# Performance work log

Measured on AMD Instinct MI355X. Metric: run time of the kernel, lower is better.

## Reference

```python
import jax, jax.numpy as jnp
import numpy as np

B, N, D, H = 128, 512, 128, 8
DK = D // H
CLIP = 10.0                      # tanh_clipping
NORM = float(np.sqrt(D))         # norm_factor = sqrt(embedding_dim), used as multiplier (as in source)


def setup_inputs() -> dict:
    key = jax.random.key(0)
    ks = jax.random.split(key, 7)
    std = float(1.0 / np.sqrt(D))
    return {
        "embeddings": jax.random.normal(ks[0], (B, N, D), dtype=jnp.float32),
        "eval_seq": jax.random.randint(ks[1], (B, N), 0, N, dtype=jnp.int32),
        "W_placeholder": jax.random.uniform(ks[2], (2 * D,), jnp.float32, -std, std),
        "W_node": jax.random.normal(ks[3], (D, 3 * D), jnp.float32) * std,
        "W_fixed": jax.random.normal(ks[4], (D, D), jnp.float32) * std,
        "W_step": jax.random.normal(ks[5], (2 * D, D), jnp.float32) * std,
        "W_out": jax.random.normal(ks[6], (D, D), jnp.float32) * std,
    }


def _decode(embeddings, eval_seq, W_placeholder, W_node, W_fixed, W_step, W_out):
    # Precomputed (fixed) projections, as in the torch module before the decode loop
    proj = embeddings @ W_node                                  # [B,N,3D]
    gK, gV, lK = jnp.split(proj, 3, axis=-1)
    gK = gK.reshape(B, N, H, DK).transpose(2, 0, 1, 3)          # [H,B,N,dk]
    gV = gV.reshape(B, N, H, DK).transpose(2, 0, 1, 3)          # [H,B,N,dk]
    fixed = embeddings.mean(axis=1) @ W_fixed                   # [B,D]
    batch_ix = jnp.arange(B)

    def step_logp(ctx, mask):
        # ctx: [B,2D] step context; mask: [B,N] bool (True = visited)
        query = fixed + ctx @ W_step                            # [B,D]
        qh = query.reshape(B, H, DK)
        compat = NORM * jnp.einsum('bhd,hbnd->hbn', qh, gK)     # [H,B,N]
        compat = jnp.where(mask[None], -jnp.inf, compat)        # mask_inner
        attn = jax.nn.softmax(compat, axis=-1)
        heads = jnp.einsum('hbn,hbnd->hbd', attn, gV)           # [H,B,dk]
        glimpse = heads.transpose(1, 0, 2).reshape(B, D) @ W_out
        logits = NORM * jnp.einsum('bnd,bd->bn', lK, glimpse)   # [B,N]
        logits = jnp.tanh(logits) * CLIP
        logits = jnp.where(mask, -jnp.inf, logits)              # mask_logits
        return jax.nn.log_softmax(logits, axis=-1)              # temp = 1.0

    # step 0: W_placeholder context, empty mask
    mask0 = jnp.zeros((B, N), dtype=bool)
    ctx0 = jnp.broadcast_to(W_placeholder[None, :], (B, 2 * D))
    lp0 = step_logp(ctx0, mask0)
    sel0 = eval_seq[:, 0]
    mask1 = mask0.at[batch_ix, sel0].set(True)
    emb_first = embeddings[batch_ix, sel0]                      # [B,D] (constant across steps)

    def body(carry, sel_i):
        mask, last = carry
        ctx = jnp.concatenate([emb_first, embeddings[batch_ix, last]], axis=-1)  # [B,2D]
        lp = step_logp(ctx, mask)
        new_mask = mask.at[batch_ix, sel_i].set(True)           # update mask AFTER computing log_p
        return (new_mask, sel_i), lp

    (_, _), lps = jax.lax.scan(body, (mask1, sel0), eval_seq[:, 1:].T)  # lps: [N-1,B,N]
    log_p = jnp.concatenate([lp0[None], lps], axis=0).transpose(1, 0, 2)  # [B,N,N]
    return log_p


def reference(embeddings, eval_seq, W_placeholder, W_node, W_fixed, W_step, W_out):
    log_p = _decode(embeddings, eval_seq, W_placeholder, W_node, W_fixed, W_step, W_out)
    return log_p, eval_seq
```

## Files before the change

### kernel.cpp

```cpp
#include <hip/hip_runtime.h>
#include <math.h>

#define B_ 128
#define N_ 512
#define D_ 128
#define H_ 8
#define NORM_ 11.313708498984761f
#define SC_ 16.322324f
#define HSC_ 32.644648f
#define CLIP_ 10.0f
#define MASKC_ -3.0e38f
#define NEG_BIG_ -1.0e30f
#define L2E_ 1.4426950408889634f
#define LN2_ 0.6931471805599453f

typedef unsigned short ushortx;
typedef __attribute__((ext_vector_type(8))) short s8v;
typedef __attribute__((ext_vector_type(4))) float f4v;

#define MFMA_ __builtin_amdgcn_mfma_f32_16x16x32_bf16

__device__ __forceinline__ unsigned short f2bf(float x) {
  union { float f; unsigned u; } v; v.f = x;
  unsigned r = v.u + 0x7fffu + ((v.u >> 16) & 1u);
  return (unsigned short)(r >> 16);
}
__device__ __forceinline__ float bf2f(ushortx u) {
  union { unsigned u; float f; } v; v.u = ((unsigned)u) << 16; return v.f;
}
__device__ __forceinline__ unsigned cvtpk(float lo, float hi) {
  unsigned r;
  asm("v_cvt_pk_bf16_f32 %0, %1, %2" : "=v"(r) : "v"(lo), "v"(hi));
  return r;
}
__device__ __forceinline__ float exp2_hw(float x) {
  float r; asm("v_exp_f32 %0, %1" : "=v"(r) : "v"(x)); return r;
}
__device__ __forceinline__ float log2_hw(float x) {
  float r; asm("v_log_f32 %0, %1" : "=v"(r) : "v"(x)); return r;
}
__device__ __forceinline__ float rcp_hw(float x) {
  float r; asm("v_rcp_f32 %0, %1" : "=v"(r) : "v"(x)); return r;
}
__device__ __forceinline__ float max3f(float a, float b, float c) {
  float r; asm("v_max3_f32 %0, %1, %2, %3" : "=v"(r) : "v"(a), "v"(b), "v"(c));
  return r;
}

__global__ __launch_bounds__(512)
void prologue(const float* __restrict__ emb, const int* __restrict__ seq,
              const float* __restrict__ Wp, const float* __restrict__ Wnode,
              const float* __restrict__ Wfix, const float* __restrict__ Wstep,
              const float* __restrict__ Wout,
              ushortx* __restrict__ WfT, ushortx* __restrict__ WsbT,
              ushortx* __restrict__ Ksrt, ushortx* __restrict__ n_orig,
              ushortx* __restrict__ Qb0, float* __restrict__ Abuf,
              float* __restrict__ out, int tail_count) {
  const int blk = blockIdx.x;
  const int t = threadIdx.x;

  if (blk < 128) {
    const int c = blk * 4 + (t >> 7);
    const int k = t & 127;
    if (c < 256) {
      WfT[c * 128 + k] = f2bf(Wnode[k * 384 + c]);
    } else if (c < 384) {
      const int d = c - 256;
      float s = 0.f;
      #pragma unroll 4
      for (int j = 0; j < 128; ++j) s += Wnode[k * 384 + 256 + j] * Wout[d * 128 + j];
      WfT[c * 128 + k] = f2bf(s);
    } else {
      const int d = c - 384;
      WsbT[d * 128 + k] = f2bf(Wstep[(128 + k) * 128 + d] * SC_);
    }
    return;
  }

  if (blk < 256) {
    const int b = blk - 128;
    const int lane = t & 63, wv = t >> 6;
    __shared__ int Tl[512];
    __shared__ int wsum[8];
    __shared__ int tot_s;

    Tl[t] = 0x7fffffff;
    __syncthreads();
    const int node = seq[b * 512 + t];
    atomicMin(&Tl[node], t + 1);
    __syncthreads();

    const int f = (Tl[node] == t + 1) ? 1 : 0;
    const unsigned long long bal = __ballot(f);
    const int excl = __popcll(bal & ((1ull << lane) - 1ull));
    if (lane == 0) wsum[wv] = __popcll(bal);
    __syncthreads();
    int woff = 0;
    #pragma unroll
    for (int i = 0; i < 8; ++i) woff += (i < wv) ? wsum[i] : 0;
    const int Kt = woff + excl;
    Ksrt[b * 512 + t] = (ushortx)Kt;
    if (f) n_orig[b * 512 + Kt] = (ushortx)node;
    if (t == 511) tot_s = Kt + f;

    const int g = (Tl[t] == 0x7fffffff) ? 1 : 0;
    const unsigned long long bal2 = __ballot(g);
    const int excl2 = __popcll(bal2 & ((1ull << lane) - 1ull));
    const int w2 = __popcll(bal2);
    __syncthreads();
    if (lane == 0) wsum[wv] = w2;
    __syncthreads();
    int woff2 = 0;
    #pragma unroll
    for (int i = 0; i < 8; ++i) woff2 += (i < wv) ? wsum[i] : 0;
    if (g) n_orig[b * 512 + tot_s + woff2 + excl2] = (ushortx)t;
    return;
  }

  if (blk < 384) {
    const int b = blk - 256;
    __shared__ float4 red4[16][33];
    __shared__ float mean[128];
    const int row0 = t >> 5, c4 = t & 31;
    const float* eb = emb + (size_t)b * 512 * 128;
    float4 acc = {0.f, 0.f, 0.f, 0.f};
    for (int it = 0; it < 32; ++it) {
      const float4 x = *(const float4*)(eb + (size_t)(it * 16 + row0) * 128 + c4 * 4);
      acc.x += x.x; acc.y += x.y; acc.z += x.z; acc.w += x.w;
    }
    red4[row0][c4] = acc;
    __syncthreads();
    if (t < 128) {
      const int c4b = t >> 2, j = t & 3;
      float s = 0.f;
      #pragma unroll
      for (int r = 0; r < 16; ++r) s += ((const float*)&red4[r][c4b])[j];
      mean[t] = s * (1.f / 512.f);
    }
    __syncthreads();
    if (t < 128) {
      float fx = 0.f;
      for (int k = 0; k < 128; ++k) fx += mean[k] * Wfix[k * 128 + t];
      float c = 0.f;
      for (int k = 0; k < 256; ++k) c += Wp[k] * Wstep[k * 128 + t];
      const int sel0 = seq[b * N_];
      const float* ef = eb + (size_t)sel0 * 128;
      float a = 0.f;
      for (int k = 0; k < 128; ++k) a += ef[k] * Wstep[k * 128 + t];
      Qb0[b * 128 + t] = f2bf((fx + c) * SC_);
      Abuf[b * 128 + t] = (fx + a) * SC_;
    }
    return;
  }

  {
    const int i = (blk - 384) * 512 + t;
    if (i < tail_count) out[(size_t)B_ * N_ * N_ + i] = (float)seq[i];
  }
}

__global__ __launch_bounds__(256)
void proj_mfma(const float* __restrict__ E, const ushortx* __restrict__ WfT,
               const ushortx* __restrict__ n_orig,
               ushortx* __restrict__ gK, ushortx* __restrict__ gVt,
               ushortx* __restrict__ lKt) {
  __shared__ ushortx S[64 * 216];
  const int tid = threadIdx.x;
  const int w = tid >> 6, l = tid & 63;
  const int m16 = l & 15, lg = l >> 4;
  const int b = blockIdx.x >> 3;
  const int n0 = (blockIdx.x & 7) * 64;
  const int p_row = n0 + w * 16 + m16;
  const int orig = (int)n_orig[b * 512 + p_row];
  const float* er = E + ((size_t)b * 512 + orig) * 128;

  s8v af[4];
  #pragma unroll
  for (int ks = 0; ks < 4; ++ks) {
    float4 f0 = *(const float4*)(er + ks * 32 + lg * 8);
    float4 f1 = *(const float4*)(er + ks * 32 + lg * 8 + 4);
    union { unsigned u[4]; s8v v; } au;
    au.u[0] = cvtpk(f0.x, f0.y); au.u[1] = cvtpk(f0.z, f0.w);
    au.u[2] = cvtpk(f1.x, f1.y); au.u[3] = cvtpk(f1.z, f1.w);
    af[ks] = au.v;
  }

  const int lrow = w * 16 + 4 * lg;
  #pragma unroll
  for (int half = 0; half < 2; ++half) {
    const int cb = half * 192;
    #pragma unroll
    for (int ct = 0; ct < 12; ++ct) {
      const int lc = ct * 16 + m16;
      f4v acc = {0.f, 0.f, 0.f, 0.f};
      #pragma unroll
      for (int ks = 0; ks < 4; ++ks) {
        const s8v bf = *(const s8v*)(WfT + (size_t)(cb + lc) * 128 + ks * 32 + lg * 8);
        acc = MFMA_(af[ks], bf, acc, 0, 0, 0);
      }
      const unsigned w01 = cvtpk(acc[0], acc[1]);
      const unsigned w23 = cvtpk(acc[2], acc[3]);
      S[(lrow + 0) * 216 + lc] = (ushortx)(w01 & 0xffffu);
      S[(lrow + 1) * 216 + lc] = (ushortx)(w01 >> 16);
      S[(lrow + 2) * 216 + lc] = (ushortx)(w23 & 0xffffu);
      S[(lrow + 3) * 216 + lc] = (ushortx)(w23 >> 16);
    }
    __syncthreads();

    if (half == 0) {
      #pragma unroll
      for (int it = 0; it < 4; ++it) {
        const int idx = it * 256 + tid;
        const int hh = idx >> 7, nn = (idx >> 1) & 63, hf = idx & 1;
        const uint4 v = *(const uint4*)(&S[nn * 216 + hh * 16 + hf * 8]);
        *(uint4*)(gK + (((size_t)(b * 8 + hh) * 512 + n0 + nn) * 16 + hf * 8)) = v;
      }
      #pragma unroll
      for (int it = 0; it < 2; ++it) {
        const int idx = it * 256 + tid;
        const int hh = idx >> 7, dk = (idx >> 3) & 15, n8 = (idx & 7) * 8;
        const int lc = 128 + hh * 16 + dk;
        unsigned wr[4];
        #pragma unroll
        for (int j = 0; j < 4; ++j)
          wr[j] = (unsigned)S[(n8 + 2 * j) * 216 + lc] |
                  ((unsigned)S[(n8 + 2 * j + 1) * 216 + lc] << 16);
        uint4 o; o.x = wr[0]; o.y = wr[1]; o.z = wr[2]; o.w = wr[3];
        *(uint4*)(gVt + (((size_t)(b * 8 + hh) * 16 + dk) * 512 + n0 + n8)) = o;
      }
    } else {
      #pragma unroll
      for (int it = 0; it < 4; ++it) {
        const int idx = it * 256 + tid;
        const int nn = idx >> 4, d8 = (idx & 15) * 8;
        const uint4 v = *(const uint4*)(&S[nn * 216 + 64 + d8]);
        *(uint4*)(lKt + ((size_t)(b * 512 + n0 + nn) * 128 + d8)) = v;
      }
      #pragma unroll
      for (int it = 0; it < 2; ++it) {
        const int idx = it * 256 + tid;
        const int hq = idx >> 7, dk = (idx >> 3) & 15, n8 = (idx & 7) * 8;
        const int lc = hq * 16 + dk;
        unsigned wr[4];
        #pragma unroll
        for (int j = 0; j < 4; ++j)
          wr[j] = (unsigned)S[(n8 + 2 * j) * 216 + lc] |
                  ((unsigned)S[(n8 + 2 * j + 1) * 216 + lc] << 16);
        uint4 o; o.x = wr[0]; o.y = wr[1]; o.z = wr[2]; o.w = wr[3];
        *(uint4*)(gVt + (((size_t)(b * 8 + 4 + hq) * 16 + dk) * 512 + n0 + n8)) = o;
      }
    }
    __syncthreads();
  }
}

__global__ __launch_bounds__(512, 8)
void decode_mfma(const ushortx* __restrict__ gK,
                 const ushortx* __restrict__ gVt,
                 const ushortx* __restrict__ lKt,
                 const float* __restrict__ emb,
                 const int* __restrict__ seq,
                 const ushortx* __restrict__ WsbT,
                 const float* __restrict__ Abuf,
                 const ushortx* __restrict__ Qb0,
                 const ushortx* __restrict__ Ksrt,
                 const ushortx* __restrict__ n_orig,
                 float* __restrict__ out) {
  const int id = blockIdx.x;
  const int xcd = id & 7, pos = id >> 3;
  const int b = xcd * 16 + (pos >> 5);
  const int s0 = (pos & 31) * 16;
  const int tid = threadIdx.x;
  const int w = tid >> 6, l = tid & 63;
  const int m16 = l & 15, lg = l >> 4;

  __shared__ ushortx logitsTb[512 * 26];
  __shared__ ushortx ctxh[16][136];
  __shared__ ushortx Qt[16][136];
  __shared__ ushortx norig_l[512];
  __shared__ ushortx Ko[16];
  __shared__ int sel_l[16];
  __shared__ float Ab[128];

  norig_l[tid] = n_orig[b * 512 + tid];
  if (tid < 16) {
    Ko[tid] = Ksrt[b * 512 + s0 + tid];
    const int sg = s0 + tid;
    sel_l[tid] = (sg >= 1) ? seq[b * 512 + sg - 1] : 0;
  }
  if (tid < 128) Ab[tid] = Abuf[b * 128 + tid];
  __syncthreads();

  if (tid < 256) {
    const int row = tid >> 4, c8 = (tid & 15) * 8;
    const float* er = emb + ((size_t)b * 512 + sel_l[row]) * 128 + c8;
    float4 f0 = *(const float4*)(er);
    float4 f1 = *(const float4*)(er + 4);
    unsigned* dst = (unsigned*)&ctxh[row][c8];
    dst[0] = cvtpk(f0.x, f0.y); dst[1] = cvtpk(f0.z, f0.w);
    dst[2] = cvtpk(f1.x, f1.y); dst[3] = cvtpk(f1.z, f1.w);
  }
  __syncthreads();

  const int h = w;
  {
    s8v aw[4];
    #pragma unroll
    for (int ks = 0; ks < 4; ++ks)
      aw[ks] = *(const s8v*)(WsbT + (size_t)(h * 16 + m16) * 128 + ks * 32 + lg * 8);
    f4v acc = {0.f, 0.f, 0.f, 0.f};
    #pragma unroll
    for (int ks = 0; ks < 4; ++ks) {
      const s8v bf = *(const s8v*)(&ctxh[m16][ks * 32 + lg * 8]);
      acc = MFMA_(aw[ks], bf, acc, 0, 0, 0);
    }
    const int d0 = h * 16 + 4 * lg;
    unsigned q01 = cvtpk(acc[0] + Ab[d0], acc[1] + Ab[d0 + 1]);
    unsigned q23 = cvtpk(acc[2] + Ab[d0 + 2], acc[3] + Ab[d0 + 3]);
    if (s0 == 0 && m16 == 0) {
      q01 = *(const unsigned*)(Qb0 + b * 128 + d0);
      q23 = *(const unsigned*)(Qb0 + b * 128 + d0 + 2);
    }
    unsigned* qdst = (unsigned*)&Qt[m16][d0];
    qdst[0] = q01; qdst[1] = q23;
  }
  __syncthreads();

  s8v qf = {};
  if (lg < 2) qf = *(const s8v*)(&Qt[m16][h * 16 + lg * 8]);

  s8v ones;
  {
    union { unsigned u[4]; s8v v; } ou;
    ou.u[0] = 0x3F803F80u; ou.u[1] = 0x3F803F80u;
    ou.u[2] = 0x3F803F80u; ou.u[3] = 0x3F803F80u;
    ones = ou.v;
  }

  const int K0i = (int)Ko[0], K15 = (int)Ko[15];
  const int chStart = K0i >> 5;
  const int chClean = (K15 + 31) >> 5;
  const int Ks = (int)Ko[m16];
  const size_t bh = (size_t)(b * 8 + h);

  f4v Oacc = {0.f, 0.f, 0.f, 0.f};
  f4v Lacc = {0.f, 0.f, 0.f, 0.f};
  float m_run = NEG_BIG_;
  const int nA0 = 8 * (m16 >> 2) + (m16 & 3);

  for (int ch = chStart; ch < 16; ++ch) {
    const int base = ch * 32;
    s8v a0 = {}, a1 = {};
    if (lg < 2) {
      a0 = *(const s8v*)(gK + ((bh * 512 + base + nA0) * 16 + lg * 8));
      a1 = *(const s8v*)(gK + ((bh * 512 + base + nA0 + 4) * 16 + lg * 8));
    }
    const s8v av = *(const s8v*)(gVt + ((bh * 16 + m16) * 512 + base + lg * 8));

    f4v z = {0.f, 0.f, 0.f, 0.f};
    f4v st0 = MFMA_(a0, qf, z, 0, 0, 0);
    f4v st1 = MFMA_(a1, qf, z, 0, 0, 0);

    float cm = max3f(st0[0], st0[1], st0[2]);
    cm = max3f(cm, st0[3], st1[0]);
    cm = max3f(cm, st1[1], st1[2]);
    cm = fmaxf(cm, st1[3]);
    cm = fmaxf(cm, __shfl_xor(cm, 16));
    cm = fmaxf(cm, __shfl_xor(cm, 32));

    if (__any(cm > m_run + 8.0f)) {
      const float mn = fmaxf(m_run, cm);
      const float cr = exp2_hw(m_run - mn);
      m_run = mn;
      Lacc[0] *= cr;
      Oacc[0] *= cr; Oacc[1] *= cr; Oacc[2] *= cr; Oacc[3] *= cr;
    }

    float p[8];
    #pragma unroll
    for (int r = 0; r < 4; ++r) {
      p[r]     = exp2_hw(st0[r] - m_run);
      p[4 + r] = exp2_hw(st1[r] - m_run);
    }
    if (ch < chClean) {
      const int nb = base + 8 * lg;
      #pragma unroll
      for (int j = 0; j < 8; ++j) p[j] = (nb + j < Ks) ? 0.f : p[j];
    }
    union { unsigned u[4]; s8v v; } pu;
    pu.u[0] = cvtpk(p[0], p[1]); pu.u[1] = cvtpk(p[2], p[3]);
    pu.u[2] = cvtpk(p[4], p[5]); pu.u[3] = cvtpk(p[6], p[7]);
    Oacc = MFMA_(av, pu.v, Oacc, 0, 0, 0);
    Lacc = MFMA_(ones, pu.v, Lacc, 0, 0, 0);
  }

  const float scale = rcp_hw(Lacc[0]) * HSC_;
  {
    const int d0 = h * 16 + 4 * lg;
    unsigned* hd = (unsigned*)&ctxh[m16][d0];
    hd[0] = cvtpk(Oacc[0] * scale, Oacc[1] * scale);
    hd[1] = cvtpk(Oacc[2] * scale, Oacc[3] * scale);
  }
  __syncthreads();

  #pragma unroll
  for (int nt = 0; nt < 4; ++nt) {
    const int n0 = w * 64 + nt * 16;
    const int pb = (n0 + 4 * lg) * 26 + m16;
    if (n0 + 16 <= K0i) {
      logitsTb[pb]      = f2bf(MASKC_);
      logitsTb[pb + 26] = f2bf(MASKC_);
      logitsTb[pb + 52] = f2bf(MASKC_);
      logitsTb[pb + 78] = f2bf(MASKC_);
      continue;
    }
    f4v acc = {0.f, 0.f, 0.f, 0.f};
    #pragma unroll
    for (int ks = 0; ks < 4; ++ks) {
      const s8v aL = *(const s8v*)(lKt + ((size_t)b * 512 + n0 + m16) * 128 + ks * 32 + lg * 8);
      const s8v bH = *(const s8v*)(&ctxh[m16][ks * 32 + lg * 8]);
      acc = MFMA_(aL, bH, acc, 0, 0, 0);
    }
    const bool bnd = (n0 < K15);
    float lgv[4];
    #pragma unroll
    for (int r = 0; r < 4; ++r) {
      const int p = n0 + 4 * lg + r;
      float x = fminf(fmaxf(acc[r], -43.f), 43.f);
      const float e2 = exp2_hw(x);
      float lv = CLIP_ * (e2 - 1.f) * rcp_hw(e2 + 1.f);
      if (bnd && p < Ks) lv = MASKC_;
      lgv[r] = lv;
    }
    const unsigned pk01 = cvtpk(lgv[0], lgv[1]);
    const unsigned pk23 = cvtpk(lgv[2], lgv[3]);
    logitsTb[pb]      = (ushortx)pk01;
    logitsTb[pb + 26] = (ushortx)(pk01 >> 16);
    logitsTb[pb + 52] = (ushortx)pk23;
    logitsTb[pb + 78] = (ushortx)(pk23 >> 16);
  }
  __syncthreads();

  int no[8];
  #pragma unroll
  for (int i = 0; i < 8; ++i) no[i] = (int)norig_l[i * 64 + l];
  #pragma unroll
  for (int pass = 0; pass < 2; ++pass) {
    const int s = w + pass * 8;
    float v[8];
    #pragma unroll
    for (int i = 0; i < 8; ++i) v[i] = bf2f(logitsTb[(i * 64 + l) * 26 + s]);
    float mm = max3f(v[0], v[1], v[2]);
    mm = max3f(mm, v[3], v[4]);
    mm = max3f(mm, v[5], v[6]);
    mm = fmaxf(mm, v[7]);
    #pragma unroll
    for (int off = 1; off <= 32; off <<= 1) mm = fmaxf(mm, __shfl_xor(mm, off));
    float es = 0.f;
    #pragma unroll
    for (int i = 0; i < 8; ++i) es += exp2_hw((v[i] - mm) * L2E_);
    #pragma unroll
    for (int off = 1; off <= 32; off <<= 1) es += __shfl_xor(es, off);
    const float logZ = mm + LN2_ * log2_hw(es);
    float* orow = out + ((size_t)(b * N_ + s0 + s)) * N_;
    #pragma unroll
    for (int i = 0; i < 8; ++i)
      orow[no[i]] = fmaxf(v[i] - logZ, NEG_BIG_);
  }
}

extern "C" void kernel_launch(void* const* d_in, const int* in_sizes, int n_in,
                              void* d_out, int out_size, void* d_ws, size_t ws_size,
                              hipStream_t stream) {
  const float* emb   = (const float*)d_in[0];
  const int*   seq   = (const int*)d_in[1];
  const float* Wp    = (const float*)d_in[2];
  const float* Wnode = (const float*)d_in[3];
  const float* Wfix  = (const float*)d_in[4];
  const float* Wstep = (const float*)d_in[5];
  const float* Wout  = (const float*)d_in[6];
  float* out = (float*)d_out;

  ushortx* gK    = (ushortx*)d_ws;
  ushortx* gVt   = gK   + (size_t)8388608;
  ushortx* lKt   = gVt  + (size_t)8388608;
  ushortx* WfT   = lKt  + (size_t)8388608;
  ushortx* WsbT  = WfT  + (size_t)49152;
  ushortx* Ksrt  = WsbT + (size_t)16384;
  ushortx* n_or  = Ksrt + (size_t)65536;
  ushortx* Qb0   = n_or + (size_t)65536;
  float*   Abuf  = (float*)(Qb0 + (size_t)16384);

  const long long lp_elems = (long long)B_ * N_ * N_;
  const int tail = (int)((long long)out_size - lp_elems);

  prologue<<<512, 512, 0, stream>>>(emb, seq, Wp, Wnode, Wfix, Wstep, Wout,
                                    WfT, WsbT, Ksrt, n_or, Qb0, Abuf,
                                    out, tail > 0 ? tail : 0);
  proj_mfma<<<1024, 256, 0, stream>>>(emb, WfT, n_or, gK, gVt, lKt);
  decode_mfma<<<4096, 512, 0, stream>>>(gK, gVt, lKt, emb, seq, WsbT, Abuf,
                                        Qb0, Ksrt, n_or, out);
}
```

Measured before the change: 238.3 us.

## Process 32 decode steps per block to reuse gK/gV/lK loads

Each decode block now handles 32 query steps instead of 16. Every gK/gVt chunk loaded in the attention loop feeds two independent online-softmax accumulators, and the lKt tiles are reused for both halves of the logits phase. This halves the grid and the global traffic for keys and values per step. In exchange each block does twice the serial work, holds more registers, uses more shared memory and adds barriers. The attention loop also starts at the first half's start chunk, so the second half loses some of the chunk skipping it had before.

After: 224.7 us, median of 3. 5.7% less time.

```diff
diff --git a/kernel.cpp b/kernel.cpp
--- a/kernel.cpp
+++ b/kernel.cpp
@@ -268,22 +268,22 @@
                  float* __restrict__ out) {
   const int id = blockIdx.x;
   const int xcd = id & 7, pos = id >> 3;
-  const int b = xcd * 16 + (pos >> 5);
-  const int s0 = (pos & 31) * 16;
+  const int b = xcd * 16 + (pos >> 4);
+  const int s0 = (pos & 15) * 32;
   const int tid = threadIdx.x;
   const int w = tid >> 6, l = tid & 63;
   const int m16 = l & 15, lg = l >> 4;
 
   __shared__ ushortx logitsTb[512 * 26];
-  __shared__ ushortx ctxh[16][136];
-  __shared__ ushortx Qt[16][136];
+  __shared__ ushortx ctxh[32][136];
+  __shared__ ushortx Qt[32][136];
   __shared__ ushortx norig_l[512];
-  __shared__ ushortx Ko[16];
-  __shared__ int sel_l[16];
+  __shared__ ushortx Ko[32];
+  __shared__ int sel_l[32];
   __shared__ float Ab[128];
 
   norig_l[tid] = n_orig[b * 512 + tid];
-  if (tid < 16) {
+  if (tid < 32) {
     Ko[tid] = Ksrt[b * 512 + s0 + tid];
     const int sg = s0 + tid;
     sel_l[tid] = (sg >= 1) ? seq[b * 512 + sg - 1] : 0;
@@ -291,7 +291,7 @@
   if (tid < 128) Ab[tid] = Abuf[b * 128 + tid];
   __syncthreads();
 
-  if (tid < 256) {
+  {
     const int row = tid >> 4, c8 = (tid & 15) * 8;
     const float* er = emb + ((size_t)b * 512 + sel_l[row]) * 128 + c8;
     float4 f0 = *(const float4*)(er);
@@ -308,26 +308,32 @@
     #pragma unroll
     for (int ks = 0; ks < 4; ++ks)
       aw[ks] = *(const s8v*)(WsbT + (size_t)(h * 16 + m16) * 128 + ks * 32 + lg * 8);
-    f4v acc = {0.f, 0.f, 0.f, 0.f};
-    #pragma unroll
-    for (int ks = 0; ks < 4; ++ks) {
-      const s8v bf = *(const s8v*)(&ctxh[m16][ks * 32 + lg * 8]);
-      acc = MFMA_(aw[ks], bf, acc, 0, 0, 0);
-    }
-    const int d0 = h * 16 + 4 * lg;
-    unsigned q01 = cvtpk(acc[0] + Ab[d0], acc[1] + Ab[d0 + 1]);
-    unsigned q23 = cvtpk(acc[2] + Ab[d0 + 2], acc[3] + Ab[d0 + 3]);
-    if (s0 == 0 && m16 == 0) {
-      q01 = *(const unsigned*)(Qb0 + b * 128 + d0);
-      q23 = *(const unsigned*)(Qb0 + b * 128 + d0 + 2);
-    }
-    unsigned* qdst = (unsigned*)&Qt[m16][d0];
-    qdst[0] = q01; qdst[1] = q23;
+    #pragma unroll
+    for (int t = 0; t < 2; ++t) {
+      f4v acc = {0.f, 0.f, 0.f, 0.f};
+      #pragma unroll
+      for (int ks = 0; ks < 4; ++ks) {
+        const s8v bf = *(const s8v*)(&ctxh[t * 16 + m16][ks * 32 + lg * 8]);
+        acc = MFMA_(aw[ks], bf, acc, 0, 0, 0);
+      }
+      const int d0 = h * 16 + 4 * lg;
+      unsigned q01 = cvtpk(acc[0] + Ab[d0], acc[1] + Ab[d0 + 1]);
+      unsigned q23 = cvtpk(acc[2] + Ab[d0 + 2], acc[3] + Ab[d0 + 3]);
+      if (s0 == 0 && t == 0 && m16 == 0) {
+        q01 = *(const unsigned*)(Qb0 + b * 128 + d0);
+        q23 = *(const unsigned*)(Qb0 + b * 128 + d0 + 2);
+      }
+      unsigned* qdst = (unsigned*)&Qt[t * 16 + m16][d0];
+      qdst[0] = q01; qdst[1] = q23;
+    }
   }
   __syncthreads();
 
-  s8v qf = {};
-  if (lg < 2) qf = *(const s8v*)(&Qt[m16][h * 16 + lg * 8]);
+  s8v qfA = {}, qfB = {};
+  if (lg < 2) {
+    qfA = *(const s8v*)(&Qt[m16][h * 16 + lg * 8]);
+    qfB = *(const s8v*)(&Qt[16 + m16][h * 16 + lg * 8]);
+  }
 
   s8v ones;
   {
@@ -337,15 +343,17 @@
     ones = ou.v;
   }
 
-  const int K0i = (int)Ko[0], K15 = (int)Ko[15];
-  const int chStart = K0i >> 5;
-  const int chClean = (K15 + 31) >> 5;
-  const int Ks = (int)Ko[m16];
+  const int K0A = (int)Ko[0], K15 = (int)Ko[15];
+  const int K0B = (int)Ko[16], K31 = (int)Ko[31];
+  const int chStart = K0A >> 5;
+  const int chCleanA = (K15 + 31) >> 5;
+  const int chCleanB = (K31 + 31) >> 5;
+  const int KsA = (int)Ko[m16], KsB = (int)Ko[16 + m16];
   const size_t bh = (size_t)(b * 8 + h);
 
-  f4v Oacc = {0.f, 0.f, 0.f, 0.f};
-  f4v Lacc = {0.f, 0.f, 0.f, 0.f};
-  float m_run = NEG_BIG_;
+  f4v OA = {0.f, 0.f, 0.f, 0.f}, OB = {0.f, 0.f, 0.f, 0.f};
+  f4v LA = {0.f, 0.f, 0.f, 0.f}, LB = {0.f, 0.f, 0.f, 0.f};
+  float mA = NEG_BIG_, mB = NEG_BIG_;
   const int nA0 = 8 * (m16 >> 2) + (m16 & 3);
 
   for (int ch = chStart; ch < 16; ++ch) {
@@ -356,116 +364,160 @@
       a1 = *(const s8v*)(gK + ((bh * 512 + base + nA0 + 4) * 16 + lg * 8));
     }
     const s8v av = *(const s8v*)(gVt + ((bh * 16 + m16) * 512 + base + lg * 8));
+    const int nb = base + 8 * lg;
 
     f4v z = {0.f, 0.f, 0.f, 0.f};
-    f4v st0 = MFMA_(a0, qf, z, 0, 0, 0);
-    f4v st1 = MFMA_(a1, qf, z, 0, 0, 0);
-
-    float cm = max3f(st0[0], st0[1], st0[2]);
-    cm = max3f(cm, st0[3], st1[0]);
-    cm = max3f(cm, st1[1], st1[2]);
-    cm = fmaxf(cm, st1[3]);
-    cm = fmaxf(cm, __shfl_xor(cm, 16));
-    cm = fmaxf(cm, __shfl_xor(cm, 32));
-
-    if (__any(cm > m_run + 8.0f)) {
-      const float mn = fmaxf(m_run, cm);
-      const float cr = exp2_hw(m_run - mn);
-      m_run = mn;
-      Lacc[0] *= cr;
-      Oacc[0] *= cr; Oacc[1] *= cr; Oacc[2] *= cr; Oacc[3] *= cr;
-    }
-
-    float p[8];
-    #pragma unroll
-    for (int r = 0; r < 4; ++r) {
-      p[r]     = exp2_hw(st0[r] - m_run);
-      p[4 + r] = exp2_hw(st1[r] - m_run);
-    }
-    if (ch < chClean) {
-      const int nb = base + 8 * lg;
-      #pragma unroll
-      for (int j = 0; j < 8; ++j) p[j] = (nb + j < Ks) ? 0.f : p[j];
-    }
-    union { unsigned u[4]; s8v v; } pu;
-    pu.u[0] = cvtpk(p[0], p[1]); pu.u[1] = cvtpk(p[2], p[3]);
-    pu.u[2] = cvtpk(p[4], p[5]); pu.u[3] = cvtpk(p[6], p[7]);
-    Oacc = MFMA_(av, pu.v, Oacc, 0, 0, 0);
-    Lacc = MFMA_(ones, pu.v, Lacc, 0, 0, 0);
-  }
-
-  const float scale = rcp_hw(Lacc[0]) * HSC_;
+    {
+      f4v st0 = MFMA_(a0, qfA, z, 0, 0, 0);
+      f4v st1 = MFMA_(a1, qfA, z, 0, 0, 0);
+      float cm = max3f(st0[0], st0[1], st0[2]);
+      cm = max3f(cm, st0[3], st1[0]);
+      cm = max3f(cm, st1[1], st1[2]);
+      cm = fmaxf(cm, st1[3]);
+      cm = fmaxf(cm, __shfl_xor(cm, 16));
+      cm = fmaxf(cm, __shfl_xor(cm, 32));
+      if (__any(cm > mA + 8.0f)) {
+        const float mn = fmaxf(mA, cm);
+        const float cr = exp2_hw(mA - mn);
+        mA = mn;
+        LA[0] *= cr;
+        OA[0] *= cr; OA[1] *= cr; OA[2] *= cr; OA[3] *= cr;
+      }
+      float p[8];
+      #pragma unroll
+      for (int r = 0; r < 4; ++r) {
+        p[r]     = exp2_hw(st0[r] - mA);
+        p[4 + r] = exp2_hw(st1[r] - mA);
+      }
+      if (ch < chCleanA) {
+        #pragma unroll
+        for (int j = 0; j < 8; ++j) p[j] = (nb + j < KsA) ? 0.f : p[j];
+      }
+      union { unsigned u[4]; s8v v; } pu;
+      pu.u[0] = cvtpk(p[0], p[1]); pu.u[1] = cvtpk(p[2], p[3]);
+      pu.u[2] = cvtpk(p[4], p[5]); pu.u[3] = cvtpk(p[6], p[7]);
+      OA = MFMA_(av, pu.v, OA, 0, 0, 0);
+      LA = MFMA_(ones, pu.v, LA, 0, 0, 0);
+    }
+    {
+      f4v st0 = MFMA_(a0, qfB, z, 0, 0, 0);
+      f4v st1 = MFMA_(a1, qfB, z, 0, 0, 0);
+      float cm = max3f(st0[0], st0[1], st0[2]);
+      cm = max3f(cm, st0[3], st1[0]);
+      cm = max3f(cm, st1[1], st1[2]);
+      cm = fmaxf(cm, st1[3]);
+      cm = fmaxf(cm, __shfl_xor(cm, 16));
+      cm = fmaxf(cm, __shfl_xor(cm, 32));
+      if (__any(cm > mB + 8.0f)) {
+        const float mn = fmaxf(mB, cm);
+        const float cr = exp2_hw(mB - mn);
+        mB = mn;
+        LB[0] *= cr;
+        OB[0] *= cr; OB[1] *= cr; OB[2] *= cr; OB[3] *= cr;
+      }
+      float p[8];
+      #pragma unroll
+      for (int r = 0; r < 4; ++r) {
+        p[r]     = exp2_hw(st0[r] - mB);
+        p[4 + r] = exp2_hw(st1[r] - mB);
+      }
+      if (ch < chCleanB) {
+        #pragma unroll
+        for (int j = 0; j < 8; ++j) p[j] = (nb + j < KsB) ? 0.f : p[j];
+      }
+      union { unsigned u[4]; s8v v; } pu;
+      pu.u[0] = cvtpk(p[0], p[1]); pu.u[1] = cvtpk(p[2], p[3]);
+      pu.u[2] = cvtpk(p[4], p[5]); pu.u[3] = cvtpk(p[6], p[7]);
+      OB = MFMA_(av, pu.v, OB, 0, 0, 0);
+      LB = MFMA_(ones, pu.v, LB, 0, 0, 0);
+    }
+  }
+
   {
+    const float scA = rcp_hw(LA[0]) * HSC_;
+    const float scB = rcp_hw(LB[0]) * HSC_;
     const int d0 = h * 16 + 4 * lg;
-    unsigned* hd = (unsigned*)&ctxh[m16][d0];
-    hd[0] = cvtpk(Oacc[0] * scale, Oacc[1] * scale);
-    hd[1] = cvtpk(Oacc[2] * scale, Oacc[3] * scale);
-  }
-  __syncthreads();
-
-  #pragma unroll
-  for (int nt = 0; nt < 4; ++nt) {
-    const int n0 = w * 64 + nt * 16;
-    const int pb = (n0 + 4 * lg) * 26 + m16;
-    if (n0 + 16 <= K0i) {
-      logitsTb[pb]      = f2bf(MASKC_);
-      logitsTb[pb + 26] = f2bf(MASKC_);
-      logitsTb[pb + 52] = f2bf(MASKC_);
-      logitsTb[pb + 78] = f2bf(MASKC_);
-      continue;
-    }
-    f4v acc = {0.f, 0.f, 0.f, 0.f};
-    #pragma unroll
-    for (int ks = 0; ks < 4; ++ks) {
-      const s8v aL = *(const s8v*)(lKt + ((size_t)b * 512 + n0 + m16) * 128 + ks * 32 + lg * 8);
-      const s8v bH = *(const s8v*)(&ctxh[m16][ks * 32 + lg * 8]);
-      acc = MFMA_(aL, bH, acc, 0, 0, 0);
-    }
-    const bool bnd = (n0 < K15);
-    float lgv[4];
-    #pragma unroll
-    for (int r = 0; r < 4; ++r) {
-      const int p = n0 + 4 * lg + r;
-      float x = fminf(fmaxf(acc[r], -43.f), 43.f);
-      const float e2 = exp2_hw(x);
-      float lv = CLIP_ * (e2 - 1.f) * rcp_hw(e2 + 1.f);
-      if (bnd && p < Ks) lv = MASKC_;
-      lgv[r] = lv;
-    }
-    const unsigned pk01 = cvtpk(lgv[0], lgv[1]);
-    const unsigned pk23 = cvtpk(lgv[2], lgv[3]);
-    logitsTb[pb]      = (ushortx)pk01;
-    logitsTb[pb + 26] = (ushortx)(pk01 >> 16);
-    logitsTb[pb + 52] = (ushortx)pk23;
-    logitsTb[pb + 78] = (ushortx)(pk23 >> 16);
+    unsigned* hdA = (unsigned*)&ctxh[m16][d0];
+    hdA[0] = cvtpk(OA[0] * scA, OA[1] * scA);
+    hdA[1] = cvtpk(OA[2] * scA, OA[3] * scA);
+    unsigned* hdB = (unsigned*)&ctxh[16 + m16][d0];
+    hdB[0] = cvtpk(OB[0] * scB, OB[1] * scB);
+    hdB[1] = cvtpk(OB[2] * scB, OB[3] * scB);
   }
   __syncthreads();
 
   int no[8];
   #pragma unroll
   for (int i = 0; i < 8; ++i) no[i] = (int)norig_l[i * 64 + l];
+
   #pragma unroll
-  for (int pass = 0; pass < 2; ++pass) {
-    const int s = w + pass * 8;
-    float v[8];
-    #pragma unroll
-    for (int i = 0; i < 8; ++i) v[i] = bf2f(logitsTb[(i * 64 + l) * 26 + s]);
-    float mm = max3f(v[0], v[1], v[2]);
-    mm = max3f(mm, v[3], v[4]);
-    mm = max3f(mm, v[5], v[6]);
-    mm = fmaxf(mm, v[7]);
-    #pragma unroll
-    for (int off = 1; off <= 32; off <<= 1) mm = fmaxf(mm, __shfl_xor(mm, off));
-    float es = 0.f;
-    #pragma unroll
-    for (int i = 0; i < 8; ++i) es += exp2_hw((v[i] - mm) * L2E_);
-    #pragma unroll
-    for (int off = 1; off <= 32; off <<= 1) es += __shfl_xor(es, off);
-    const float logZ = mm + LN2_ * log2_hw(es);
-    float* orow = out + ((size_t)(b * N_ + s0 + s)) * N_;
-    #pragma unroll
-    for (int i = 0; i < 8; ++i)
-      orow[no[i]] = fmaxf(v[i] - logZ, NEG_BIG_);
+  for (int half = 0; half < 2; ++half) {
+    const int K0h = half ? K0B : K0A;
+    const int K15h = half ? K31 : K15;
+    const int Ksh = half ? KsB : KsA;
+
+    #pragma unroll
+    for (int nt = 0; nt < 4; ++nt) {
+      const int n0 = w * 64 + nt * 16;
+      const int pb = (n0 + 4 * lg) * 26 + m16;
+      if (n0 + 16 <= K0h) {
+        logitsTb[pb]      = f2bf(MASKC_);
+        logitsTb[pb + 26] = f2bf(MASKC_);
+        logitsTb[pb + 52] = f2bf(MASKC_);
+        logitsTb[pb + 78] = f2bf(MASKC_);
+        continue;
+      }
+      f4v acc = {0.f, 0.f, 0.f, 0.f};
+      #pragma unroll
+      for (int ks = 0; ks < 4; ++ks) {
+        const s8v aL = *(const s8v*)(lKt + ((size_t)b * 512 + n0 + m16) * 128 + ks * 32 + lg * 8);
+        const s8v bH = *(const s8v*)(&ctxh[half * 16 + m16][ks * 32 + lg * 8]);
+        acc = MFMA_(aL, bH, acc, 0, 0, 0);
+      }
+      const bool bnd = (n0 < K15h);
+      float lgv[4];
+      #pragma unroll
+      for (int r = 0; r < 4; ++r) {
+        const int p = n0 + 4 * lg + r;
+        float x = fminf(fmaxf(acc[r], -43.f), 43.f);
+        const float e2 = exp2_hw(x);
+        float lv = CLIP_ * (e2 - 1.f) * rcp_hw(e2 + 1.f);
+        if (bnd && p < Ksh) lv = MASKC_;
+        lgv[r] = lv;
+      }
+      const unsigned pk01 = cvtpk(lgv[0], lgv[1]);
+      const unsigned pk23 = cvtpk(lgv[2], lgv[3]);
+      logitsTb[pb]      = (ushortx)pk01;
+      logitsTb[pb + 26] = (ushortx)(pk01 >> 16);
+      logitsTb[pb + 52] = (ushortx)pk23;
+      logitsTb[pb + 78] = (ushortx)(pk23 >> 16);
+    }
+    __syncthreads();
+
+    #pragma unroll
+    for (int pass = 0; pass < 2; ++pass) {
+      const int s = w + pass * 8;
+      float v[8];
+      #pragma unroll
+      for (int i = 0; i < 8; ++i) v[i] = bf2f(logitsTb[(i * 64 + l) * 26 + s]);
+      float mm = max3f(v[0], v[1], v[2]);
+      mm = max3f(mm, v[3], v[4]);
+      mm = max3f(mm, v[5], v[6]);
+      mm = fmaxf(mm, v[7]);
+      #pragma unroll
+      for (int off = 1; off <= 32; off <<= 1) mm = fmaxf(mm, __shfl_xor(mm, off));
+      float es = 0.f;
+      #pragma unroll
+      for (int i = 0; i < 8; ++i) es += exp2_hw((v[i] - mm) * L2E_);
+      #pragma unroll
+      for (int off = 1; off <= 32; off <<= 1) es += __shfl_xor(es, off);
+      const float logZ = mm + LN2_ * log2_hw(es);
+      float* orow = out + ((size_t)(b * N_ + s0 + half * 16 + s)) * N_;
+      #pragma unroll
+      for (int i = 0; i < 8; ++i)
+        orow[no[i]] = fmaxf(v[i] - logZ, NEG_BIG_);
+    }
+    __syncthreads();
   }
 }
 
@@ -498,6 +550,6 @@
                                     WfT, WsbT, Ksrt, n_or, Qb0, Abuf,
                                     out, tail > 0 ? tail : 0);
   proj_mfma<<<1024, 256, 0, stream>>>(emb, WfT, n_or, gK, gVt, lKt);
-  decode_mfma<<<4096, 512, 0, stream>>>(gK, gVt, lKt, emb, seq, WsbT, Abuf,
+  decode_mfma<<<2048, 512, 0, stream>>>(gK, gVt, lKt, emb, seq, WsbT, Abuf,
                                         Qb0, Ksrt, n_or, out);
 }
```

## Process 64 decode steps per block to reuse gK/gV/lK loads

Applied to the files above, without the earlier changes.

Each decode block now handles 64 query steps (four 16-step tiles) instead of 16, so the key/value chunk loads in the attention loop and the lK loads in the logits stage are shared across four tiles. The grid shrinks from 4096 to 1024 blocks and launch bounds drop to 4 blocks per CU to allow more registers for the four sets of accumulators. The trade-off is more register pressure, fewer blocks for latency hiding, and chStart taken from the first tile, which makes later tiles process chunks they could have skipped.

After: 229.2 us. 1.04x faster.

```diff
diff --git a/kernel.cpp b/kernel.cpp
--- a/kernel.cpp
+++ b/kernel.cpp
@@ -254,7 +254,7 @@
   }
 }
 
-__global__ __launch_bounds__(512, 8)
+__global__ __launch_bounds__(512, 4)
 void decode_mfma(const ushortx* __restrict__ gK,
                  const ushortx* __restrict__ gVt,
                  const ushortx* __restrict__ lKt,
@@ -268,22 +268,22 @@
                  float* __restrict__ out) {
   const int id = blockIdx.x;
   const int xcd = id & 7, pos = id >> 3;
-  const int b = xcd * 16 + (pos >> 5);
-  const int s0 = (pos & 31) * 16;
+  const int b = xcd * 16 + (pos >> 3);
+  const int s0 = (pos & 7) * 64;
   const int tid = threadIdx.x;
   const int w = tid >> 6, l = tid & 63;
   const int m16 = l & 15, lg = l >> 4;
 
   __shared__ ushortx logitsTb[512 * 26];
-  __shared__ ushortx ctxh[16][136];
-  __shared__ ushortx Qt[16][136];
+  __shared__ ushortx ctxh[64][136];
+  __shared__ ushortx Qt[64][136];
   __shared__ ushortx norig_l[512];
-  __shared__ ushortx Ko[16];
-  __shared__ int sel_l[16];
+  __shared__ ushortx Ko[64];
+  __shared__ int sel_l[64];
   __shared__ float Ab[128];
 
   norig_l[tid] = n_orig[b * 512 + tid];
-  if (tid < 16) {
+  if (tid < 64) {
     Ko[tid] = Ksrt[b * 512 + s0 + tid];
     const int sg = s0 + tid;
     sel_l[tid] = (sg >= 1) ? seq[b * 512 + sg - 1] : 0;
@@ -291,8 +291,9 @@
   if (tid < 128) Ab[tid] = Abuf[b * 128 + tid];
   __syncthreads();
 
-  if (tid < 256) {
-    const int row = tid >> 4, c8 = (tid & 15) * 8;
+  #pragma unroll
+  for (int rr = 0; rr < 2; ++rr) {
+    const int row = rr * 32 + (tid >> 4), c8 = (tid & 15) * 8;
     const float* er = emb + ((size_t)b * 512 + sel_l[row]) * 128 + c8;
     float4 f0 = *(const float4*)(er);
     float4 f1 = *(const float4*)(er + 4);
@@ -308,26 +309,34 @@
     #pragma unroll
     for (int ks = 0; ks < 4; ++ks)
       aw[ks] = *(const s8v*)(WsbT + (size_t)(h * 16 + m16) * 128 + ks * 32 + lg * 8);
-    f4v acc = {0.f, 0.f, 0.f, 0.f};
-    #pragma unroll
-    for (int ks = 0; ks < 4; ++ks) {
-      const s8v bf = *(const s8v*)(&ctxh[m16][ks * 32 + lg * 8]);
-      acc = MFMA_(aw[ks], bf, acc, 0, 0, 0);
-    }
-    const int d0 = h * 16 + 4 * lg;
-    unsigned q01 = cvtpk(acc[0] + Ab[d0], acc[1] + Ab[d0 + 1]);
-    unsigned q23 = cvtpk(acc[2] + Ab[d0 + 2], acc[3] + Ab[d0 + 3]);
-    if (s0 == 0 && m16 == 0) {
-      q01 = *(const unsigned*)(Qb0 + b * 128 + d0);
-      q23 = *(const unsigned*)(Qb0 + b * 128 + d0 + 2);
-    }
-    unsigned* qdst = (unsigned*)&Qt[m16][d0];
-    qdst[0] = q01; qdst[1] = q23;
+    #pragma unroll
+    for (int t = 0; t < 4; ++t) {
+      f4v acc = {0.f, 0.f, 0.f, 0.f};
+      #pragma unroll
+      for (int ks = 0; ks < 4; ++ks) {
+        const s8v bf = *(const s8v*)(&ctxh[t * 16 + m16][ks * 32 + lg * 8]);
+        acc = MFMA_(aw[ks], bf, acc, 0, 0, 0);
+      }
+      const int d0 = h * 16 + 4 * lg;
+      unsigned q01 = cvtpk(acc[0] + Ab[d0], acc[1] + Ab[d0 + 1]);
+      unsigned q23 = cvtpk(acc[2] + Ab[d0 + 2], acc[3] + Ab[d0 + 3]);
+      if (s0 == 0 && t == 0 && m16 == 0) {
+        q01 = *(const unsigned*)(Qb0 + b * 128 + d0);
+        q23 = *(const unsigned*)(Qb0 + b * 128 + d0 + 2);
+      }
+      unsigned* qdst = (unsigned*)&Qt[t * 16 + m16][d0];
+      qdst[0] = q01; qdst[1] = q23;
+    }
   }
   __syncthreads();
 
-  s8v qf = {};
-  if (lg < 2) qf = *(const s8v*)(&Qt[m16][h * 16 + lg * 8]);
+  s8v qf[4];
+  #pragma unroll
+  for (int t = 0; t < 4; ++t) {
+    s8v q = {};
+    if (lg < 2) q = *(const s8v*)(&Qt[t * 16 + m16][h * 16 + lg * 8]);
+    qf[t] = q;
+  }
 
   s8v ones;
   {
@@ -337,15 +346,24 @@
     ones = ou.v;
   }
 
-  const int K0i = (int)Ko[0], K15 = (int)Ko[15];
-  const int chStart = K0i >> 5;
-  const int chClean = (K15 + 31) >> 5;
-  const int Ks = (int)Ko[m16];
+  int K0_[4], K15_[4], Ks_[4], chClean_[4];
+  #pragma unroll
+  for (int t = 0; t < 4; ++t) {
+    K0_[t] = (int)Ko[t * 16];
+    K15_[t] = (int)Ko[t * 16 + 15];
+    Ks_[t] = (int)Ko[t * 16 + m16];
+    chClean_[t] = (K15_[t] + 31) >> 5;
+  }
+  const int chStart = K0_[0] >> 5;
   const size_t bh = (size_t)(b * 8 + h);
 
-  f4v Oacc = {0.f, 0.f, 0.f, 0.f};
-  f4v Lacc = {0.f, 0.f, 0.f, 0.f};
-  float m_run = NEG_BIG_;
+  f4v O[4], Lc[4];
+  float mr[4];
+  #pragma unroll
+  for (int t = 0; t < 4; ++t) {
+    f4v zz = {0.f, 0.f, 0.f, 0.f};
+    O[t] = zz; Lc[t] = zz; mr[t] = NEG_BIG_;
+  }
   const int nA0 = 8 * (m16 >> 2) + (m16 & 3);
 
   for (int ch = chStart; ch < 16; ++ch) {
@@ -356,116 +374,128 @@
       a1 = *(const s8v*)(gK + ((bh * 512 + base + nA0 + 4) * 16 + lg * 8));
     }
     const s8v av = *(const s8v*)(gVt + ((bh * 16 + m16) * 512 + base + lg * 8));
+    const int nb = base + 8 * lg;
 
     f4v z = {0.f, 0.f, 0.f, 0.f};
-    f4v st0 = MFMA_(a0, qf, z, 0, 0, 0);
-    f4v st1 = MFMA_(a1, qf, z, 0, 0, 0);
-
-    float cm = max3f(st0[0], st0[1], st0[2]);
-    cm = max3f(cm, st0[3], st1[0]);
-    cm = max3f(cm, st1[1], st1[2]);
-    cm = fmaxf(cm, st1[3]);
-    cm = fmaxf(cm, __shfl_xor(cm, 16));
-    cm = fmaxf(cm, __shfl_xor(cm, 32));
-
-    if (__any(cm > m_run + 8.0f)) {
-      const float mn = fmaxf(m_run, cm);
-      const float cr = exp2_hw(m_run - mn);
-      m_run = mn;
-      Lacc[0] *= cr;
-      Oacc[0] *= cr; Oacc[1] *= cr; Oacc[2] *= cr; Oacc[3] *= cr;
-    }
-
-    float p[8];
-    #pragma unroll
-    for (int r = 0; r < 4; ++r) {
-      p[r]     = exp2_hw(st0[r] - m_run);
-      p[4 + r] = exp2_hw(st1[r] - m_run);
-    }
-    if (ch < chClean) {
-      const int nb = base + 8 * lg;
-      #pragma unroll
-      for (int j = 0; j < 8; ++j) p[j] = (nb + j < Ks) ? 0.f : p[j];
-    }
-    union { unsigned u[4]; s8v v; } pu;
-    pu.u[0] = cvtpk(p[0], p[1]); pu.u[1] = cvtpk(p[2], p[3]);
-    pu.u[2] = cvtpk(p[4], p[5]); pu.u[3] = cvtpk(p[6], p[7]);
-    Oacc = MFMA_(av, pu.v, Oacc, 0, 0, 0);
-    Lacc = MFMA_(ones, pu.v, Lacc, 0, 0, 0);
-  }
-
-  const float scale = rcp_hw(Lacc[0]) * HSC_;
+    #pragma unroll
+    for (int t = 0; t < 4; ++t) {
+      f4v st0 = MFMA_(a0, qf[t], z, 0, 0, 0);
+      f4v st1 = MFMA_(a1, qf[t], z, 0, 0, 0);
+      float cm = max3f(st0[0], st0[1], st0[2]);
+      cm = max3f(cm, st0[3], st1[0]);
+      cm = max3f(cm, st1[1], st1[2]);
+      cm = fmaxf(cm, st1[3]);
+      cm = fmaxf(cm, __shfl_xor(cm, 16));
+      cm = fmaxf(cm, __shfl_xor(cm, 32));
+      if (__any(cm > mr[t] + 8.0f)) {
+        const float mn = fmaxf(mr[t], cm);
+        const float cr = exp2_hw(mr[t] - mn);
+        mr[t] = mn;
+        Lc[t][0] *= cr;
+        O[t][0] *= cr; O[t][1] *= cr; O[t][2] *= cr; O[t][3] *= cr;
+      }
+      float p[8];
+      #pragma unroll
+      for (int r = 0; r < 4; ++r) {
+        p[r]     = exp2_hw(st0[r] - mr[t]);
+        p[4 + r] = exp2_hw(st1[r] - mr[t]);
+      }
+      if (ch < chClean_[t]) {
+        #pragma unroll
+        for (int j = 0; j < 8; ++j) p[j] = (nb + j < Ks_[t]) ? 0.f : p[j];
+      }
+      union { unsigned u[4]; s8v v; } pu;
+      pu.u[0] = cvtpk(p[0], p[1]); pu.u[1] = cvtpk(p[2], p[3]);
+      pu.u[2] = cvtpk(p[4], p[5]); pu.u[3] = cvtpk(p[6], p[7]);
+      O[t] = MFMA_(av, pu.v, O[t], 0, 0, 0);
+      Lc[t] = MFMA_(ones, pu.v, Lc[t], 0, 0, 0);
+    }
+  }
+
   {
     const int d0 = h * 16 + 4 * lg;
-    unsigned* hd = (unsigned*)&ctxh[m16][d0];
-    hd[0] = cvtpk(Oacc[0] * scale, Oacc[1] * scale);
-    hd[1] = cvtpk(Oacc[2] * scale, Oacc[3] * scale);
+    #pragma unroll
+    for (int t = 0; t < 4; ++t) {
+      const float sc = rcp_hw(Lc[t][0]) * HSC_;
+      unsigned* hd = (unsigned*)&ctxh[t * 16 + m16][d0];
+      hd[0] = cvtpk(O[t][0] * sc, O[t][1] * sc);
+      hd[1] = cvtpk(O[t][2] * sc, O[t][3] * sc);
+    }
   }
   __syncthreads();
 
-  #pragma unroll
-  for (int nt = 0; nt < 4; ++nt) {
-    const int n0 = w * 64 + nt * 16;
-    const int pb = (n0 + 4 * lg) * 26 + m16;
-    if (n0 + 16 <= K0i) {
-      logitsTb[pb]      = f2bf(MASKC_);
-      logitsTb[pb + 26] = f2bf(MASKC_);
-      logitsTb[pb + 52] = f2bf(MASKC_);
-      logitsTb[pb + 78] = f2bf(MASKC_);
-      continue;
-    }
-    f4v acc = {0.f, 0.f, 0.f, 0.f};
-    #pragma unroll
-    for (int ks = 0; ks < 4; ++ks) {
-      const s8v aL = *(const s8v*)(lKt + ((size_t)b * 512 + n0 + m16) * 128 + ks * 32 + lg * 8);
-      const s8v bH = *(const s8v*)(&ctxh[m16][ks * 32 + lg * 8]);
-      acc = MFMA_(aL, bH, acc, 0, 0, 0);
-    }
-    const bool bnd = (n0 < K15);
-    float lgv[4];
-    #pragma unroll
-    for (int r = 0; r < 4; ++r) {
-      const int p = n0 + 4 * lg + r;
-      float x = fminf(fmaxf(acc[r], -43.f), 43.f);
-      const float e2 = exp2_hw(x);
-      float lv = CLIP_ * (e2 - 1.f) * rcp_hw(e2 + 1.f);
-      if (bnd && p < Ks) lv = MASKC_;
-      lgv[r] = lv;
-    }
-    const unsigned pk01 = cvtpk(lgv[0], lgv[1]);
-    const unsigned pk23 = cvtpk(lgv[2], lgv[3]);
-    logitsTb[pb]      = (ushortx)pk01;
-    logitsTb[pb + 26] = (ushortx)(pk01 >> 16);
-    logitsTb[pb + 52] = (ushortx)pk23;
-    logitsTb[pb + 78] = (ushortx)(pk23 >> 16);
-  }
-  __syncthreads();
-
   int no[8];
   #pragma unroll
   for (int i = 0; i < 8; ++i) no[i] = (int)norig_l[i * 64 + l];
-  #pragma unroll
-  for (int pass = 0; pass < 2; ++pass) {
-    const int s = w + pass * 8;
-    float v[8];
-    #pragma unroll
-    for (int i = 0; i < 8; ++i) v[i] = bf2f(logitsTb[(i * 64 + l) * 26 + s]);
-    float mm = max3f(v[0], v[1], v[2]);
-    mm = max3f(mm, v[3], v[4]);
-    mm = max3f(mm, v[5], v[6]);
-    mm = fmaxf(mm, v[7]);
-    #pragma unroll
-    for (int off = 1; off <= 32; off <<= 1) mm = fmaxf(mm, __shfl_xor(mm, off));
-    float es = 0.f;
-    #pragma unroll
-    for (int i = 0; i < 8; ++i) es += exp2_hw((v[i] - mm) * L2E_);
-    #pragma unroll
-    for (int off = 1; off <= 32; off <<= 1) es += __shfl_xor(es, off);
-    const float logZ = mm + LN2_ * log2_hw(es);
-    float* orow = out + ((size_t)(b * N_ + s0 + s)) * N_;
-    #pragma unroll
-    for (int i = 0; i < 8; ++i)
-      orow[no[i]] = fmaxf(v[i] - logZ, NEG_BIG_);
+
+  #pragma unroll
+  for (int half = 0; half < 4; ++half) {
+    const int K0h = K0_[half];
+    const int K15h = K15_[half];
+    const int Ksh = Ks_[half];
+
+    #pragma unroll
+    for (int nt = 0; nt < 4; ++nt) {
+      const int n0 = w * 64 + nt * 16;
+      const int pb = (n0 + 4 * lg) * 26 + m16;
+      if (n0 + 16 <= K0h) {
+        logitsTb[pb]      = f2bf(MASKC_);
+        logitsTb[pb + 26] = f2bf(MASKC_);
+        logitsTb[pb + 52] = f2bf(MASKC_);
+        logitsTb[pb + 78] = f2bf(MASKC_);
+        continue;
+      }
+      f4v acc = {0.f, 0.f, 0.f, 0.f};
+      #pragma unroll
+      for (int ks = 0; ks < 4; ++ks) {
+        const s8v aL = *(const s8v*)(lKt + ((size_t)b * 512 + n0 + m16) * 128 + ks * 32 + lg * 8);
+        const s8v bH = *(const s8v*)(&ctxh[half * 16 + m16][ks * 32 + lg * 8]);
+        acc = MFMA_(aL, bH, acc, 0, 0, 0);
+      }
+      const bool bnd = (n0 < K15h);
+      float lgv[4];
+      #pragma unroll
+      for (int r = 0; r < 4; ++r) {
+        const int p = n0 + 4 * lg + r;
+        float x = fminf(fmaxf(acc[r], -43.f), 43.f);
+        const float e2 = exp2_hw(x);
+        float lv = CLIP_ * (e2 - 1.f) * rcp_hw(e2 + 1.f);
+        if (bnd && p < Ksh) lv = MASKC_;
+        lgv[r] = lv;
+      }
+      const unsigned pk01 = cvtpk(lgv[0], lgv[1]);
+      const unsigned pk23 = cvtpk(lgv[2], lgv[3]);
+      logitsTb[pb]      = (ushortx)pk01;
+      logitsTb[pb + 26] = (ushortx)(pk01 >> 16);
+      logitsTb[pb + 52] = (ushortx)pk23;
+      logitsTb[pb + 78] = (ushortx)(pk23 >> 16);
+    }
+    __syncthreads();
+
+    #pragma unroll
+    for (int pass = 0; pass < 2; ++pass) {
+      const int s = w + pass * 8;
+      float v[8];
+      #pragma unroll
+      for (int i = 0; i < 8; ++i) v[i] = bf2f(logitsTb[(i * 64 + l) * 26 + s]);
+      float mm = max3f(v[0], v[1], v[2]);
+      mm = max3f(mm, v[3], v[4]);
+      mm = max3f(mm, v[5], v[6]);
+      mm = fmaxf(mm, v[7]);
+      #pragma unroll
+      for (int off = 1; off <= 32; off <<= 1) mm = fmaxf(mm, __shfl_xor(mm, off));
+      float es = 0.f;
+      #pragma unroll
+      for (int i = 0; i < 8; ++i) es += exp2_hw((v[i] - mm) * L2E_);
+      #pragma unroll
+      for (int off = 1; off <= 32; off <<= 1) es += __shfl_xor(es, off);
+      const float logZ = mm + LN2_ * log2_hw(es);
+      float* orow = out + ((size_t)(b * N_ + s0 + half * 16 + s)) * N_;
+      #pragma unroll
+      for (int i = 0; i < 8; ++i)
+        orow[no[i]] = fmaxf(v[i] - logZ, NEG_BIG_);
+    }
+    __syncthreads();
   }
 }
 
@@ -498,6 +528,6 @@
                                     WfT, WsbT, Ksrt, n_or, Qb0, Abuf,
                                     out, tail > 0 ? tail : 0);
   proj_mfma<<<1024, 256, 0, stream>>>(emb, WfT, n_or, gK, gVt, lKt);
-  decode_mfma<<<4096, 512, 0, stream>>>(gK, gVt, lKt, emb, seq, WsbT, Abuf,
+  decode_mfma<<<1024, 512, 0, stream>>>(gK, gVt, lKt, emb, seq, WsbT, Abuf,
                                         Qb0, Ksrt, n_or, out);
 }
```
